# Performance work log

Hardware: AMD Instinct MI355X
Metric: run time of the kernel (lower is better)

The kernel has to match this reference:

```python
import jax, jax.numpy as jnp
import numpy as np

D_MODEL = 128
N_LAYERS = 2
D_STATE = 16
D_CONV = 4
EXPAND = 2
GRID = 16
D_INNER = D_MODEL * EXPAND
DT_RANK = (D_MODEL + 15) // 16  # mamba_ssm default: ceil(d_model/16) = 8
BATCH = 128
SEQ = 200


def setup_inputs() -> dict:
    key = jax.random.key(0)
    ks = jax.random.split(key, 24)
    L = N_LAYERS

    def rn(k, shape, scale=0.02):
        return jax.random.normal(k, shape, dtype=jnp.float32) * scale

    A_init = jnp.log(jnp.broadcast_to(
        jnp.arange(1, D_STATE + 1, dtype=jnp.float32), (L, D_INNER, D_STATE)))
    kan_scale = 1.0 / (np.sqrt(D_MODEL) * np.sqrt(GRID))
    return {
        "x": jax.random.normal(ks[0], (BATCH, SEQ, D_MODEL), dtype=jnp.float32),
        "in_w": rn(ks[1], (L, 2 * D_INNER, D_MODEL)),
        "out_w": rn(ks[2], (L, D_MODEL, D_INNER)),
        "conv_w_f": rn(ks[3], (L, D_INNER, D_CONV), 0.1),
        "conv_b_f": rn(ks[4], (L, D_INNER), 0.01),
        "conv_w_b": rn(ks[5], (L, D_INNER, D_CONV), 0.1),
        "conv_b_b": rn(ks[6], (L, D_INNER), 0.01),
        "xproj_w_f": rn(ks[7], (L, DT_RANK + 2 * D_STATE, D_INNER)),
        "xproj_w_b": rn(ks[8], (L, DT_RANK + 2 * D_STATE, D_INNER)),
        "dtproj_w_f": rn(ks[9], (L, D_INNER, DT_RANK), 0.1),
        "dtproj_b_f": rn(ks[10], (L, D_INNER), 0.01),
        "dtproj_w_b": rn(ks[11], (L, D_INNER, DT_RANK), 0.1),
        "dtproj_b_b": rn(ks[12], (L, D_INNER), 0.01),
        "A_log_f": A_init,
        "A_log_b": A_init,
        "D_f": jnp.ones((L, D_INNER), jnp.float32),
        "D_b": jnp.ones((L, D_INNER), jnp.float32),
        "ln1_w": jnp.ones((L, D_MODEL), jnp.float32),
        "ln1_b": jnp.zeros((L, D_MODEL), jnp.float32),
        "ln_w": jnp.ones((L, D_MODEL), jnp.float32),
        "ln_b": jnp.zeros((L, D_MODEL), jnp.float32),
        "kan_coef": jax.random.normal(ks[13], (L, 2, D_MODEL, D_MODEL, GRID), dtype=jnp.float32) * kan_scale,
    }


def _ln(x, w, b, eps=1e-12):
    u = x.mean(-1, keepdims=True)
    s = ((x - u) ** 2).mean(-1, keepdims=True)
    return w * (x - u) / jnp.sqrt(s + eps) + b


def _silu(x):
    return x * jax.nn.sigmoid(x)


def _mamba(x, in_w, out_w, conv_w, conv_b, xp_w, dt_w, dt_b, A_log, Dp):
    # x: (B, L, d_model). Faithful to mamba_ssm Mamba (bias=False proj, conv_bias=True).
    B, L, _ = x.shape
    xz = jnp.einsum('bld,ed->ble', x, in_w)          # (B, L, 2*d_inner)
    xi, z = jnp.split(xz, 2, axis=-1)
    # causal depthwise conv over L
    xp = jnp.pad(xi, ((0, 0), (D_CONV - 1, 0), (0, 0)))
    xc = sum(xp[:, k:k + L, :] * conv_w[:, k] for k in range(D_CONV)) + conv_b
    xc = _silu(xc)                                    # (B, L, d_inner)
    dbl = jnp.einsum('ble,fe->blf', xc, xp_w)         # (B, L, dt_rank+2*d_state)
    dt = jax.nn.softplus(
        jnp.einsum('blr,dr->bld', dbl[..., :DT_RANK], dt_w) + dt_b)
    Bm = dbl[..., DT_RANK:DT_RANK + D_STATE]          # (B, L, d_state)
    Cm = dbl[..., DT_RANK + D_STATE:]
    A = -jnp.exp(A_log)                               # (d_inner, d_state)

    def step(h, inp):
        dt_t, u_t, b_t, c_t = inp                     # (B,di),(B,di),(B,ds),(B,ds)
        h = jnp.exp(dt_t[:, :, None] * A) * h + (dt_t * u_t)[:, :, None] * b_t[:, None, :]
        return h, jnp.einsum('bds,bs->bd', h, c_t)

    h0 = jnp.zeros((B, D_INNER, D_STATE), x.dtype)
    _, ys = jax.lax.scan(step, h0, (jnp.moveaxis(dt, 1, 0), jnp.moveaxis(xc, 1, 0),
                                    jnp.moveaxis(Bm, 1, 0), jnp.moveaxis(Cm, 1, 0)))
    y = jnp.moveaxis(ys, 0, 1) + xc * Dp              # (B, L, d_inner)
    y = y * _silu(z)
    return jnp.einsum('ble,de->bld', y, out_w)


def _kan(x, coef):
    # coef: (2, outdim, inputdim, grid)
    shp = x.shape
    xf = x.reshape(-1, shp[-1])                       # (N, d)
    kk = jnp.arange(1, GRID + 1, dtype=x.dtype)
    ang = xf[:, :, None] * kk                         # (N, d, grid)
    y = (jnp.einsum('nig,jig->nj', jnp.cos(ang), coef[0])
         + jnp.einsum('nig,jig->nj', jnp.sin(ang), coef[1]))
    return y.reshape(shp[:-1] + (coef.shape[1],))


def reference(x, in_w, out_w, conv_w_f, conv_b_f, conv_w_b, conv_b_b,
              xproj_w_f, xproj_w_b, dtproj_w_f, dtproj_b_f, dtproj_w_b, dtproj_b_b,
              A_log_f, A_log_b, D_f, D_b, ln1_w, ln1_b, ln_w, ln_b, kan_coef):
    feats = []
    h = x
    for l in range(N_LAYERS):
        o = _ln(h, ln1_w[l], ln1_b[l])
        f = _mamba(o, in_w[l], out_w[l], conv_w_f[l], conv_b_f[l],
                   xproj_w_f[l], dtproj_w_f[l], dtproj_b_f[l], A_log_f[l], D_f[l])
        b = _mamba(o[:, ::-1], in_w[l], out_w[l], conv_w_b[l], conv_b_b[l],
                   xproj_w_b[l], dtproj_w_b[l], dtproj_b_b[l], A_log_b[l], D_b[l])[:, ::-1]
        o = _ln(f + b, ln_w[l], ln_b[l])
        o = _kan(o, kan_coef[l])  # dropout p=0.0 (eval) -> identity
        h = o + h
        feats.append(h)
    return sum(feats) / len(feats)
```

## Files before the change

kernel.cpp:

```cpp
#include <hip/hip_runtime.h>
#include <hip/hip_bf16.h>
#include <cmath>

#define BATCH 128
#define SEQ 200
#define DMODEL 128
#define DINNER 256
#define DSTATE 16
#define NTOK (BATCH * SEQ)

typedef __bf16 bf16x8 __attribute__((ext_vector_type(8)));
typedef float f32x4 __attribute__((ext_vector_type(4)));

__device__ __forceinline__ unsigned short f2bf(float f) {
  union { float f; unsigned u; } x{f};
  const unsigned r = x.u + 0x7fffu + ((x.u >> 16) & 1u);
  return (unsigned short)(r >> 16);
}
__device__ __forceinline__ float bf2f(unsigned short h) {
  union { unsigned u; float f; } x{(unsigned)h << 16};
  return x.f;
}
__device__ __forceinline__ void split2(float a, float b, unsigned& hp, unsigned& lp) {
  const unsigned short ha = f2bf(a), hb = f2bf(b);
  const float ra = a - bf2f(ha), rb = b - bf2f(hb);
  hp = (unsigned)ha | ((unsigned)hb << 16);
  lp = (unsigned)f2bf(ra) | ((unsigned)f2bf(rb) << 16);
}

template <int CTRL>
__device__ __forceinline__ float dpp_add(float v) {
  const int r = __builtin_amdgcn_update_dpp(0, __float_as_int(v), CTRL, 0xF, 0xF, true);
  return v + __int_as_float(r);
}

__device__ __forceinline__ float silu_f(float x) {
  return x / (1.f + __expf(-x));
}

__global__ __launch_bounds__(256) void ln_kernel(const float* __restrict__ in,
                                                 const float* __restrict__ w,
                                                 const float* __restrict__ b,
                                                 float* __restrict__ out) {
  const int wv = threadIdx.x >> 6;
  const int lane = threadIdx.x & 63;
  const int row = blockIdx.x * 4 + wv;
  const float2 v = *(const float2*)(in + (size_t)row * DMODEL + lane * 2);
  float s = v.x + v.y;
#pragma unroll
  for (int o = 32; o; o >>= 1) s += __shfl_xor(s, o, 64);
  const float u = s * (1.f / 128.f);
  const float dx = v.x - u, dy = v.y - u;
  float sq = dx * dx + dy * dy;
#pragma unroll
  for (int o = 32; o; o >>= 1) sq += __shfl_xor(sq, o, 64);
  const float inv = rsqrtf(sq * (1.f / 128.f) + 1e-12f);
  const float2 wv2 = *(const float2*)(w + lane * 2);
  const float2 bv2 = *(const float2*)(b + lane * 2);
  float2 o2v;
  o2v.x = fmaf(wv2.x, dx * inv, bv2.x);
  o2v.y = fmaf(wv2.y, dy * inv, bv2.y);
  *(float2*)(out + (size_t)row * DMODEL + lane * 2) = o2v;
}

__global__ __launch_bounds__(256) void wprep(const float* __restrict__ in_w,
                                             const float* __restrict__ xpwf,
                                             const float* __restrict__ xpwb,
                                             const float* __restrict__ out_w,
                                             unsigned short* __restrict__ iwH,
                                             unsigned short* __restrict__ iwL,
                                             unsigned short* __restrict__ xfH,
                                             unsigned short* __restrict__ xfL,
                                             unsigned short* __restrict__ xbH,
                                             unsigned short* __restrict__ xbL,
                                             unsigned short* __restrict__ owH,
                                             unsigned short* __restrict__ owL) {
  const int idx = blockIdx.x * 256 + threadIdx.x;
  float w;
  unsigned short *H, *L;
  int off;
  if (idx < 65536)      { w = in_w[idx];        H = iwH; L = iwL; off = idx; }
  else if (idx < 75776) { w = xpwf[idx - 65536]; H = xfH; L = xfL; off = idx - 65536; }
  else if (idx < 86016) { w = xpwb[idx - 75776]; H = xbH; L = xbL; off = idx - 75776; }
  else                  { w = out_w[idx - 86016]; H = owH; L = owL; off = idx - 86016; }
  const unsigned short h = f2bf(w);
  H[off] = h;
  L[off] = f2bf(w - bf2f(h));
}

template <int MODE>
__global__ __launch_bounds__(256) void gemm_c(const float* __restrict__ A1,
                                              const float* __restrict__ A2,
                                              const float* __restrict__ Zp,
                                              const unsigned short* __restrict__ Whi,
                                              const unsigned short* __restrict__ Wlo,
                                              float* __restrict__ C,
                                              int M, int N, int K) {
  __shared__ unsigned short AshH[64 * 40], AshL[64 * 40];
  __shared__ unsigned short BshH[128 * 40], BshL[128 * 40];
  const int tid = threadIdx.x;
  const int m0 = blockIdx.y * 64;
  const int n0 = blockIdx.x * 128;
  const int lane = tid & 63;
  const int wid = tid >> 6;
  const int arow = lane & 15;
  const int kch = (lane >> 4) * 8;
  const int bcol = wid * 32 + (lane & 15);
  f32x4 acc[4][2] = {};
  for (int k0 = 0; k0 < K; k0 += 32) {
    __syncthreads();
    {
      const int row = tid >> 2;
      const int koff = (tid & 3) * 8;
      const int m = m0 + row;
      float4 v0 = *(const float4*)(A1 + (size_t)m * K + k0 + koff);
      float4 v1 = *(const float4*)(A1 + (size_t)m * K + k0 + koff + 4);
      if (MODE == 1) {
        const float4 u0 = *(const float4*)(A2 + (size_t)m * K + k0 + koff);
        const float4 u1 = *(const float4*)(A2 + (size_t)m * K + k0 + koff + 4);
        const float4 z0 = *(const float4*)(Zp + (size_t)m * 512 + k0 + koff);
        const float4 z1 = *(const float4*)(Zp + (size_t)m * 512 + k0 + koff + 4);
        v0.x = (v0.x + u0.x) * silu_f(z0.x);
        v0.y = (v0.y + u0.y) * silu_f(z0.y);
        v0.z = (v0.z + u0.z) * silu_f(z0.z);
        v0.w = (v0.w + u0.w) * silu_f(z0.w);
        v1.x = (v1.x + u1.x) * silu_f(z1.x);
        v1.y = (v1.y + u1.y) * silu_f(z1.y);
        v1.z = (v1.z + u1.z) * silu_f(z1.z);
        v1.w = (v1.w + u1.w) * silu_f(z1.w);
      }
      unsigned h0, l0, h1, l1, h2, l2, h3, l3;
      split2(v0.x, v0.y, h0, l0);
      split2(v0.z, v0.w, h1, l1);
      split2(v1.x, v1.y, h2, l2);
      split2(v1.z, v1.w, h3, l3);
      *(uint4*)&AshH[row * 40 + koff] = make_uint4(h0, h1, h2, h3);
      *(uint4*)&AshL[row * 40 + koff] = make_uint4(l0, l1, l2, l3);
    }
    {
      const int row = tid >> 1;
      const int koff = (tid & 1) * 16;
      const int n = n0 + row;
      uint4 wh0 = make_uint4(0, 0, 0, 0), wh1 = wh0, wl0 = wh0, wl1 = wh0;
      if (n < N) {
        wh0 = *(const uint4*)(Whi + (size_t)n * K + k0 + koff);
        wh1 = *(const uint4*)(Whi + (size_t)n * K + k0 + koff + 8);
        wl0 = *(const uint4*)(Wlo + (size_t)n * K + k0 + koff);
        wl1 = *(const uint4*)(Wlo + (size_t)n * K + k0 + koff + 8);
      }
      *(uint4*)&BshH[row * 40 + koff] = wh0;
      *(uint4*)&BshH[row * 40 + koff + 8] = wh1;
      *(uint4*)&BshL[row * 40 + koff] = wl0;
      *(uint4*)&BshL[row * 40 + koff + 8] = wl1;
    }
    __syncthreads();
    const bf16x8 bh0 = *(const bf16x8*)&BshH[bcol * 40 + kch];
    const bf16x8 bh1 = *(const bf16x8*)&BshH[(bcol + 16) * 40 + kch];
    const bf16x8 bl0 = *(const bf16x8*)&BshL[bcol * 40 + kch];
    const bf16x8 bl1 = *(const bf16x8*)&BshL[(bcol + 16) * 40 + kch];
#pragma unroll
    for (int g = 0; g < 4; ++g) {
      const bf16x8 ah = *(const bf16x8*)&AshH[(g * 16 + arow) * 40 + kch];
      const bf16x8 al = *(const bf16x8*)&AshL[(g * 16 + arow) * 40 + kch];
      acc[g][0] = __builtin_amdgcn_mfma_f32_16x16x32_bf16(ah, bh0, acc[g][0], 0, 0, 0);
      acc[g][0] = __builtin_amdgcn_mfma_f32_16x16x32_bf16(al, bh0, acc[g][0], 0, 0, 0);
      acc[g][0] = __builtin_amdgcn_mfma_f32_16x16x32_bf16(ah, bl0, acc[g][0], 0, 0, 0);
      acc[g][1] = __builtin_amdgcn_mfma_f32_16x16x32_bf16(ah, bh1, acc[g][1], 0, 0, 0);
      acc[g][1] = __builtin_amdgcn_mfma_f32_16x16x32_bf16(al, bh1, acc[g][1], 0, 0, 0);
      acc[g][1] = __builtin_amdgcn_mfma_f32_16x16x32_bf16(ah, bl1, acc[g][1], 0, 0, 0);
    }
  }
  const int q0 = (lane >> 4) * 4;
#pragma unroll
  for (int g = 0; g < 4; ++g)
#pragma unroll
    for (int fc = 0; fc < 2; ++fc)
#pragma unroll
      for (int q = 0; q < 4; ++q) {
        const int m = m0 + g * 16 + q0 + q;
        const int n = n0 + wid * 32 + fc * 16 + (lane & 15);
        if (n < N) C[(size_t)m * N + n] = acc[g][fc][q];
      }
}

__global__ __launch_bounds__(256) void conv_silu_kernel(const float* __restrict__ xz,
                                                        const float* __restrict__ cwf,
                                                        const float* __restrict__ cbf,
                                                        const float* __restrict__ cwb,
                                                        const float* __restrict__ cbb,
                                                        float* __restrict__ xcf,
                                                        float* __restrict__ xcb) {
  const int n = blockIdx.x;
  const int l = n % SEQ;
  const int e = threadIdx.x;
  const float4 wf = *(const float4*)(cwf + e * 4);
  const float4 wb = *(const float4*)(cwb + e * 4);
  const float* base = xz + (size_t)n * 512 + e;
  const float wfk[4] = {wf.x, wf.y, wf.z, wf.w};
  const float wbk[4] = {wb.x, wb.y, wb.z, wb.w};
  float af = cbf[e];
#pragma unroll
  for (int k = 0; k < 4; ++k) {
    const int ll = l - 3 + k;
    if (ll >= 0) af = fmaf(wfk[k], base[(k - 3) * 512], af);
  }
  float ab = cbb[e];
#pragma unroll
  for (int k = 0; k < 4; ++k) {
    const int ll = l + 3 - k;
    if (ll < SEQ) ab = fmaf(wbk[k], base[(3 - k) * 512], ab);
  }
  xcf[(size_t)n * DINNER + e] = silu_f(af);
  xcb[(size_t)n * DINNER + e] = silu_f(ab);
}

__global__ __launch_bounds__(256) void dtsp_kernel2(const float* __restrict__ dblF,
                                                    const float* __restrict__ dblB,
                                                    const float* __restrict__ dtwF,
                                                    const float* __restrict__ dtbF,
                                                    const float* __restrict__ dtwB,
                                                    const float* __restrict__ dtbB,
                                                    float* __restrict__ dtF,
                                                    float* __restrict__ dtB) {
  const int bwd = blockIdx.y;
  const float* __restrict__ dbl = bwd ? dblB : dblF;
  const float* __restrict__ dtw = bwd ? dtwB : dtwF;
  const float* __restrict__ dtb = bwd ? dtbB : dtbF;
  float* __restrict__ dt = bwd ? dtB : dtF;
  __shared__ float r[8];
  const int n = blockIdx.x;
  const int d = threadIdx.x;
  if (threadIdx.x < 8) r[threadIdx.x] = dbl[(size_t)n * 40 + threadIdx.x];
  __syncthreads();
  const float4 w0 = *(const float4*)(dtw + d * 8);
  const float4 w1 = *(const float4*)(dtw + d * 8 + 4);
  float acc = dtb[d];
  acc += r[0] * w0.x + r[1] * w0.y + r[2] * w0.z + r[3] * w0.w;
  acc += r[4] * w1.x + r[5] * w1.y + r[6] * w1.z + r[7] * w1.w;
  const float sp = acc > 20.f ? acc : log1pf(__expf(acc));
  dt[(size_t)n * DINNER + d] = sp;
}

__global__ __launch_bounds__(256) void scan_kernel3(
    const float* __restrict__ dtF, float* xcF, const float* __restrict__ dblF,
    const float* __restrict__ AlogF, const float* __restrict__ DF,
    const float* __restrict__ dtB, float* xcB, const float* __restrict__ dblB,
    const float* __restrict__ AlogB, const float* __restrict__ DB) {
  const int bwd = blockIdx.z;
  const float* __restrict__ dt = bwd ? dtB : dtF;
  float* xc = bwd ? xcB : xcF;
  const float* __restrict__ dbl = bwd ? dblB : dblF;
  const float* __restrict__ Alog = bwd ? AlogB : AlogF;
  const float* __restrict__ Dp = bwd ? DB : DF;
  const int bb = blockIdx.y;
  const int lane = threadIdx.x & 63;
  const int wid = threadIdx.x >> 6;
  const int q = lane & 3;
  const int dl = lane >> 2;
  const int d = blockIdx.x * 64 + wid * 16 + dl;
  const float LOG2E = 1.44269504f;
  const float4 al = *(const float4*)(Alog + d * DSTATE + q * 4);
  const float4 A2 = make_float4(-__expf(al.x) * LOG2E, -__expf(al.y) * LOG2E,
                                -__expf(al.z) * LOG2E, -__expf(al.w) * LOG2E);
  const float Dd = Dp[d];
  const int t0 = bwd ? (SEQ - 1) : 0;
  const ptrdiff_t sX = bwd ? -DINNER : DINNER;
  const ptrdiff_t sB = bwd ? -40 : 40;
  const float* pdt = dt + (size_t)(bb * SEQ + t0) * DINNER + d;
  float* pxc = xc + (size_t)(bb * SEQ + t0) * DINNER + d;
  const float* pbc = dbl + (size_t)(bb * SEQ + t0) * 40 + 8 + q * 4;
  float4 h = make_float4(0.f, 0.f, 0.f, 0.f);
#pragma unroll 2
  for (int t = 0; t < SEQ; ++t) {
    const float dtv = *pdt;
    const float u = *pxc;
    const float4 Bv = *(const float4*)pbc;
    const float4 Cv = *(const float4*)(pbc + 16);
    const float du = dtv * u;
    float4 a;
    a.x = exp2f(dtv * A2.x);
    a.y = exp2f(dtv * A2.y);
    a.z = exp2f(dtv * A2.z);
    a.w = exp2f(dtv * A2.w);
    h.x = fmaf(a.x, h.x, du * Bv.x);
    h.y = fmaf(a.y, h.y, du * Bv.y);
    h.z = fmaf(a.z, h.z, du * Bv.z);
    h.w = fmaf(a.w, h.w, du * Bv.w);
    float pp = fmaf(h.w, Cv.w, fmaf(h.z, Cv.z, fmaf(h.y, Cv.y, h.x * Cv.x)));
    pp = dpp_add<0xB1>(pp);
    pp = dpp_add<0x4E>(pp);
    if (q == 0) *pxc = fmaf(u, Dd, pp);
    pdt += sX;
    pxc += sX;
    pbc += sB;
  }
}

__global__ __launch_bounds__(256) void kan_prep(const float* __restrict__ coef,
                                                unsigned short* __restrict__ Wt) {
  const int idx = blockIdx.x * 256 + threadIdx.x;
  const int k = idx & 31;
  const int j = (idx >> 5) & 127;
  const int i = idx >> 12;
  const int c = k >> 4, g = k & 15;
  Wt[idx] = f2bf(coef[(((size_t)c * 128 + j) * 128 + i) * 16 + g]);
}

__global__ __launch_bounds__(256) void kan_mfma(const float* __restrict__ x,
                                                const unsigned short* __restrict__ Wt,
                                                const float* __restrict__ hin,
                                                float* __restrict__ hout,
                                                float* __restrict__ accum,
                                                int first) {
  __shared__ float Xs[128 * 32];
  __shared__ unsigned short F[2][32 * 40];
  __shared__ unsigned short Wsh[2][128 * 40];
  const int tid = threadIdx.x;
  const int n0 = blockIdx.x * 32;
  const int wid = tid >> 6;
  const int lane = tid & 63;
  {
    const int tok = tid & 31;
    const int cq = tid >> 5;
#pragma unroll
    for (int r = 0; r < 4; ++r) {
      const int i0 = (cq + r * 8) * 4;
      const float4 v = *(const float4*)(x + (size_t)(n0 + tok) * 128 + i0);
      Xs[(i0 + 0) * 32 + tok] = v.x;
      Xs[(i0 + 1) * 32 + tok] = v.y;
      Xs[(i0 + 2) * 32 + tok] = v.z;
      Xs[(i0 + 3) * 32 + tok] = v.w;
    }
  }
  const int fn = tid >> 3;
  const int ft = tid & 7;
  const float g0 = (float)(2 * ft + 1);
  const int arow = lane & 15;
  const int kch = (lane >> 4) * 8;
  const int bcol = wid * 32 + (lane & 15);
  const int ws = tid >> 7;
  const int wrow = tid & 127;
  f32x4 acc[2][2] = {};
  for (int ii = 0; ii < 128; ii += 2) {
    __syncthreads();
    {
      const uint4* src = (const uint4*)(Wt + (size_t)(ii + ws) * 4096 + wrow * 32);
      uint4* dst = (uint4*)&Wsh[ws][wrow * 40];
      dst[0] = src[0]; dst[1] = src[1]; dst[2] = src[2]; dst[3] = src[3];
    }
#pragma unroll
    for (int s = 0; s < 2; ++s) {
      const float xv = Xs[(ii + s) * 32 + fn];
      const float y1 = xv * g0;
      const float y2 = y1 + xv;
      const float cg = __cosf(y1), sg = __sinf(y1);
      const float cg2 = __cosf(y2), sg2 = __sinf(y2);
      unsigned int* Fu = (unsigned int*)F[s];
      Fu[fn * 20 + ft] = (unsigned)f2bf(cg) | ((unsigned)f2bf(cg2) << 16);
      Fu[fn * 20 + 8 + ft] = (unsigned)f2bf(sg) | ((unsigned)f2bf(sg2) << 16);
    }
    __syncthreads();
#pragma unroll
    for (int s = 0; s < 2; ++s) {
      const bf16x8 a0 = *(const bf16x8*)&F[s][arow * 40 + kch];
      const bf16x8 a1 = *(const bf16x8*)&F[s][(16 + arow) * 40 + kch];
      const bf16x8 b0 = *(const bf16x8*)&Wsh[s][bcol * 40 + kch];
      const bf16x8 b1 = *(const bf16x8*)&Wsh[s][(bcol + 16) * 40 + kch];
      acc[0][0] = __builtin_amdgcn_mfma_f32_16x16x32_bf16(a0, b0, acc[0][0], 0, 0, 0);
      acc[1][0] = __builtin_amdgcn_mfma_f32_16x16x32_bf16(a1, b0, acc[1][0], 0, 0, 0);
      acc[0][1] = __builtin_amdgcn_mfma_f32_16x16x32_bf16(a0, b1, acc[0][1], 0, 0, 0);
      acc[1][1] = __builtin_amdgcn_mfma_f32_16x16x32_bf16(a1, b1, acc[1][1], 0, 0, 0);
    }
  }
  const int q0 = (lane >> 4) * 4;
#pragma unroll
  for (int fr = 0; fr < 2; ++fr)
#pragma unroll
    for (int fc = 0; fc < 2; ++fc)
#pragma unroll
      for (int q = 0; q < 4; ++q) {
        const int n = n0 + fr * 16 + q0 + q;
        const int j = wid * 32 + fc * 16 + (lane & 15);
        const size_t off = (size_t)n * 128 + j;
        const float v = acc[fr][fc][q] + hin[off];
        hout[off] = v;
        const float a = 0.5f * v;
        accum[off] = first ? a : (accum[off] + a);
      }
}

extern "C" void kernel_launch(void* const* d_in, const int* in_sizes, int n_in,
                              void* d_out, int out_size, void* d_ws, size_t ws_size,
                              hipStream_t stream) {
  (void)in_sizes; (void)n_in; (void)out_size;
  const float* x     = (const float*)d_in[0];
  const float* in_w  = (const float*)d_in[1];
  const float* out_w = (const float*)d_in[2];
  const float* cwf   = (const float*)d_in[3];
  const float* cbf   = (const float*)d_in[4];
  const float* cwb   = (const float*)d_in[5];
  const float* cbb   = (const float*)d_in[6];
  const float* xpwf  = (const float*)d_in[7];
  const float* xpwb  = (const float*)d_in[8];
  const float* dtwf  = (const float*)d_in[9];
  const float* dtbf  = (const float*)d_in[10];
  const float* dtwb  = (const float*)d_in[11];
  const float* dtbb  = (const float*)d_in[12];
  const float* Alogf = (const float*)d_in[13];
  const float* Alogb = (const float*)d_in[14];
  const float* Dfp   = (const float*)d_in[15];
  const float* Dbp   = (const float*)d_in[16];
  const float* ln1w  = (const float*)d_in[17];
  const float* ln1b  = (const float*)d_in[18];
  const float* lnw   = (const float*)d_in[19];
  const float* lnb   = (const float*)d_in[20];
  const float* kanc  = (const float*)d_in[21];
  float* outp = (float*)d_out;

  int C = 128;
  while (C > 8) {
    const size_t need = ((size_t)380928 + (size_t)2000 * C * SEQ) * 4;
    if (need <= ws_size) break;
    C >>= 1;
  }
  const int T = C * SEQ;

  float* p = (float*)d_ws;
  unsigned short* Wt  = (unsigned short*)p; p += 262144;
  unsigned short* iwH = (unsigned short*)p; p += 32768;
  unsigned short* iwL = (unsigned short*)p; p += 32768;
  unsigned short* xfH = (unsigned short*)p; p += 5120;
  unsigned short* xfL = (unsigned short*)p; p += 5120;
  unsigned short* xbH = (unsigned short*)p; p += 5120;
  unsigned short* xbL = (unsigned short*)p; p += 5120;
  unsigned short* owH = (unsigned short*)p; p += 16384;
  unsigned short* owL = (unsigned short*)p; p += 16384;
  float* o1   = p; p += (size_t)T * 128;
  float* xzb  = p; p += (size_t)T * 512;
  float* xcf  = p; p += (size_t)T * 256;
  float* xcb  = p; p += (size_t)T * 256;
  float* dblf = p; p += (size_t)T * 40;
  float* dblb = p; p += (size_t)T * 40;
  float* dtf  = p; p += (size_t)T * 256;
  float* dtb  = p; p += (size_t)T * 256;
  float* o2   = p; p += (size_t)T * 128;
  float* hbuf = p; p += (size_t)T * 128;

  for (int b0 = 0; b0 < BATCH; b0 += C) {
    const size_t tok0 = (size_t)b0 * SEQ;
    for (int l = 0; l < 2; ++l) {
      const float* hin = (l == 0) ? (x + tok0 * 128) : hbuf;
      wprep<<<464, 256, 0, stream>>>(in_w + (size_t)l * 65536, xpwf + (size_t)l * 10240,
                                     xpwb + (size_t)l * 10240, out_w + (size_t)l * 32768,
                                     iwH, iwL, xfH, xfL, xbH, xbL, owH, owL);
      kan_prep<<<2048, 256, 0, stream>>>(kanc + (size_t)l * 2 * 128 * 128 * 16, Wt);
      ln_kernel<<<T / 4, 256, 0, stream>>>(hin, ln1w + l * 128, ln1b + l * 128, o1);
      gemm_c<0><<<dim3(4, T / 64), 256, 0, stream>>>(o1, (const float*)nullptr,
                                                     (const float*)nullptr,
                                                     iwH, iwL, xzb, T, 512, 128);
      conv_silu_kernel<<<T, 256, 0, stream>>>(xzb, cwf + l * 1024, cbf + l * 256,
                                              cwb + l * 1024, cbb + l * 256, xcf, xcb);
      gemm_c<0><<<dim3(1, T / 64), 256, 0, stream>>>(xcf, (const float*)nullptr,
                                                     (const float*)nullptr,
                                                     xfH, xfL, dblf, T, 40, 256);
      gemm_c<0><<<dim3(1, T / 64), 256, 0, stream>>>(xcb, (const float*)nullptr,
                                                     (const float*)nullptr,
                                                     xbH, xbL, dblb, T, 40, 256);
      dtsp_kernel2<<<dim3(T, 2), 256, 0, stream>>>(dblf, dblb,
                                                   dtwf + l * 2048, dtbf + l * 256,
                                                   dtwb + l * 2048, dtbb + l * 256,
                                                   dtf, dtb);
      scan_kernel3<<<dim3(4, C, 2), 256, 0, stream>>>(
          dtf, xcf, dblf, Alogf + l * 4096, Dfp + l * 256,
          dtb, xcb, dblb, Alogb + l * 4096, Dbp + l * 256);
      gemm_c<1><<<dim3(1, T / 64), 256, 0, stream>>>(xcf, xcb, xzb + 256,
                                                     owH, owL, o1, T, 128, 256);
      ln_kernel<<<T / 4, 256, 0, stream>>>(o1, lnw + l * 128, lnb + l * 128, o2);
      kan_mfma<<<T / 32, 256, 0, stream>>>(o2, Wt, hin, hbuf,
                                           outp + tok0 * 128, l == 0 ? 1 : 0);
    }
  }
}
```

Measured before the change: 764.7 us.

## Hoist weight prep, merge x_proj GEMMs, batch conv/dt tokens, widen KAN tiles

Weight splitting and KAN coefficient prep now run once per layer outside the batch-chunk loop, with per-layer buffers. The two x_proj GEMMs are merged into one launch selected by blockIdx.z. The conv and dt-softplus kernels each handle 8 tokens per block, and the conv kernel uses a sliding window. The KAN MFMA kernel doubles its token tile to 64 and builds its cos/sin harmonics by angle-addition recurrence instead of direct sin/cos calls. The workspace layout is reworked, which leaves dead pointer setup code and raises the workspace requirement.

```diff
diff --git a/kernel.cpp b/kernel.cpp
--- a/kernel.cpp
+++ b/kernel.cpp
@@ -95,9 +95,17 @@
                                               const unsigned short* __restrict__ Whi,
                                               const unsigned short* __restrict__ Wlo,
                                               float* __restrict__ C,
+                                              const unsigned short* __restrict__ Whi2,
+                                              const unsigned short* __restrict__ Wlo2,
+                                              float* __restrict__ C2,
                                               int M, int N, int K) {
   __shared__ unsigned short AshH[64 * 40], AshL[64 * 40];
   __shared__ unsigned short BshH[128 * 40], BshL[128 * 40];
+  const float* Ause = A1;
+  const unsigned short* WH = Whi;
+  const unsigned short* WL = Wlo;
+  float* Cuse = C;
+  if (MODE == 2 && blockIdx.z == 1) { Ause = A2; WH = Whi2; WL = Wlo2; Cuse = C2; }
   const int tid = threadIdx.x;
   const int m0 = blockIdx.y * 64;
   const int n0 = blockIdx.x * 128;
@@ -113,8 +121,8 @@
       const int row = tid >> 2;
       const int koff = (tid & 3) * 8;
       const int m = m0 + row;
-      float4 v0 = *(const float4*)(A1 + (size_t)m * K + k0 + koff);
-      float4 v1 = *(const float4*)(A1 + (size_t)m * K + k0 + koff + 4);
+      float4 v0 = *(const float4*)(Ause + (size_t)m * K + k0 + koff);
+      float4 v1 = *(const float4*)(Ause + (size_t)m * K + k0 + koff + 4);
       if (MODE == 1) {
         const float4 u0 = *(const float4*)(A2 + (size_t)m * K + k0 + koff);
         const float4 u1 = *(const float4*)(A2 + (size_t)m * K + k0 + koff + 4);
@@ -143,10 +151,10 @@
       const int n = n0 + row;
       uint4 wh0 = make_uint4(0, 0, 0, 0), wh1 = wh0, wl0 = wh0, wl1 = wh0;
       if (n < N) {
-        wh0 = *(const uint4*)(Whi + (size_t)n * K + k0 + koff);
-        wh1 = *(const uint4*)(Whi + (size_t)n * K + k0 + koff + 8);
-        wl0 = *(const uint4*)(Wlo + (size_t)n * K + k0 + koff);
-        wl1 = *(const uint4*)(Wlo + (size_t)n * K + k0 + koff + 8);
+        wh0 = *(const uint4*)(WH + (size_t)n * K + k0 + koff);
+        wh1 = *(const uint4*)(WH + (size_t)n * K + k0 + koff + 8);
+        wl0 = *(const uint4*)(WL + (size_t)n * K + k0 + koff);
+        wl1 = *(const uint4*)(WL + (size_t)n * K + k0 + koff + 8);
       }
       *(uint4*)&BshH[row * 40 + koff] = wh0;
       *(uint4*)&BshH[row * 40 + koff + 8] = wh1;
@@ -179,7 +187,7 @@
       for (int q = 0; q < 4; ++q) {
         const int m = m0 + g * 16 + q0 + q;
         const int n = n0 + wid * 32 + fc * 16 + (lane & 15);
-        if (n < N) C[(size_t)m * N + n] = acc[g][fc][q];
+        if (n < N) Cuse[(size_t)m * N + n] = acc[g][fc][q];
       }
 }
 
@@ -190,28 +198,30 @@
                                                         const float* __restrict__ cbb,
                                                         float* __restrict__ xcf,
                                                         float* __restrict__ xcb) {
-  const int n = blockIdx.x;
-  const int l = n % SEQ;
+  const int n0 = blockIdx.x * 8;
+  const int l0 = n0 % SEQ;
   const int e = threadIdx.x;
   const float4 wf = *(const float4*)(cwf + e * 4);
   const float4 wb = *(const float4*)(cwb + e * 4);
-  const float* base = xz + (size_t)n * 512 + e;
-  const float wfk[4] = {wf.x, wf.y, wf.z, wf.w};
-  const float wbk[4] = {wb.x, wb.y, wb.z, wb.w};
-  float af = cbf[e];
-#pragma unroll
-  for (int k = 0; k < 4; ++k) {
-    const int ll = l - 3 + k;
-    if (ll >= 0) af = fmaf(wfk[k], base[(k - 3) * 512], af);
-  }
-  float ab = cbb[e];
-#pragma unroll
-  for (int k = 0; k < 4; ++k) {
-    const int ll = l + 3 - k;
-    if (ll < SEQ) ab = fmaf(wbk[k], base[(3 - k) * 512], ab);
-  }
-  xcf[(size_t)n * DINNER + e] = silu_f(af);
-  xcb[(size_t)n * DINNER + e] = silu_f(ab);
+  const float bfv = cbf[e], bbv = cbb[e];
+  const float* px = xz + (size_t)n0 * 512 + e;
+  float w[7];
+#pragma unroll
+  for (int j = 0; j < 6; ++j) {
+    const int l = l0 - 3 + j;
+    w[j] = (l >= 0 && l < SEQ) ? px[(j - 3) * 512] : 0.f;
+  }
+#pragma unroll
+  for (int t = 0; t < 8; ++t) {
+    const int l = l0 + t;
+    w[6] = (l + 3 < SEQ) ? px[(t + 3) * 512] : 0.f;
+    const float af = fmaf(wf.x, w[0], fmaf(wf.y, w[1], fmaf(wf.z, w[2], fmaf(wf.w, w[3], bfv))));
+    const float ab = fmaf(wb.x, w[6], fmaf(wb.y, w[5], fmaf(wb.z, w[4], fmaf(wb.w, w[3], bbv))));
+    xcf[(size_t)(n0 + t) * DINNER + e] = silu_f(af);
+    xcb[(size_t)(n0 + t) * DINNER + e] = silu_f(ab);
+#pragma unroll
+    for (int j = 0; j < 6; ++j) w[j] = w[j + 1];
+  }
 }
 
 __global__ __launch_bounds__(256) void dtsp_kernel2(const float* __restrict__ dblF,
@@ -227,18 +237,25 @@
   const float* __restrict__ dtw = bwd ? dtwB : dtwF;
   const float* __restrict__ dtb = bwd ? dtbB : dtbF;
   float* __restrict__ dt = bwd ? dtB : dtF;
-  __shared__ float r[8];
-  const int n = blockIdx.x;
+  __shared__ float r[8][8];
+  const int n0 = blockIdx.x * 8;
   const int d = threadIdx.x;
-  if (threadIdx.x < 8) r[threadIdx.x] = dbl[(size_t)n * 40 + threadIdx.x];
-  __syncthreads();
+  if (threadIdx.x < 64) {
+    const int tt = threadIdx.x >> 3, j = threadIdx.x & 7;
+    r[tt][j] = dbl[(size_t)(n0 + tt) * 40 + j];
+  }
   const float4 w0 = *(const float4*)(dtw + d * 8);
   const float4 w1 = *(const float4*)(dtw + d * 8 + 4);
-  float acc = dtb[d];
-  acc += r[0] * w0.x + r[1] * w0.y + r[2] * w0.z + r[3] * w0.w;
-  acc += r[4] * w1.x + r[5] * w1.y + r[6] * w1.z + r[7] * w1.w;
-  const float sp = acc > 20.f ? acc : log1pf(__expf(acc));
-  dt[(size_t)n * DINNER + d] = sp;
+  const float bd = dtb[d];
+  __syncthreads();
+#pragma unroll
+  for (int tt = 0; tt < 8; ++tt) {
+    float acc = bd;
+    acc += r[tt][0] * w0.x + r[tt][1] * w0.y + r[tt][2] * w0.z + r[tt][3] * w0.w;
+    acc += r[tt][4] * w1.x + r[tt][5] * w1.y + r[tt][6] * w1.z + r[tt][7] * w1.w;
+    const float sp = acc > 20.f ? acc : log1pf(__expf(acc));
+    dt[(size_t)(n0 + tt) * DINNER + d] = sp;
+  }
 }
 
 __global__ __launch_bounds__(256) void scan_kernel3(
@@ -312,77 +329,85 @@
                                                 float* __restrict__ hout,
                                                 float* __restrict__ accum,
                                                 int first) {
-  __shared__ float Xs[128 * 32];
-  __shared__ unsigned short F[2][32 * 40];
+  __shared__ float Xs[128 * 64];
+  __shared__ unsigned short F[2][64 * 40];
   __shared__ unsigned short Wsh[2][128 * 40];
   const int tid = threadIdx.x;
-  const int n0 = blockIdx.x * 32;
+  const int n0 = blockIdx.x * 64;
   const int wid = tid >> 6;
   const int lane = tid & 63;
   {
-    const int tok = tid & 31;
-    const int cq = tid >> 5;
-#pragma unroll
-    for (int r = 0; r < 4; ++r) {
-      const int i0 = (cq + r * 8) * 4;
+    const int tok = tid & 63;
+    const int cq = tid >> 6;
+#pragma unroll
+    for (int r = 0; r < 8; ++r) {
+      const int i0 = cq * 32 + r * 4;
       const float4 v = *(const float4*)(x + (size_t)(n0 + tok) * 128 + i0);
-      Xs[(i0 + 0) * 32 + tok] = v.x;
-      Xs[(i0 + 1) * 32 + tok] = v.y;
-      Xs[(i0 + 2) * 32 + tok] = v.z;
-      Xs[(i0 + 3) * 32 + tok] = v.w;
-    }
-  }
-  const int fn = tid >> 3;
-  const int ft = tid & 7;
-  const float g0 = (float)(2 * ft + 1);
+      Xs[(i0 + 0) * 64 + tok] = v.x;
+      Xs[(i0 + 1) * 64 + tok] = v.y;
+      Xs[(i0 + 2) * 64 + tok] = v.z;
+      Xs[(i0 + 3) * 64 + tok] = v.w;
+    }
+  }
+  const int fs = tid >> 7;
+  const int fn = (tid & 127) >> 1;
+  const int fh = tid & 1;
+  const int wrow = tid & 127;
   const int arow = lane & 15;
   const int kch = (lane >> 4) * 8;
   const int bcol = wid * 32 + (lane & 15);
-  const int ws = tid >> 7;
-  const int wrow = tid & 127;
-  f32x4 acc[2][2] = {};
+  f32x4 acc[4][2] = {};
   for (int ii = 0; ii < 128; ii += 2) {
     __syncthreads();
     {
-      const uint4* src = (const uint4*)(Wt + (size_t)(ii + ws) * 4096 + wrow * 32);
-      uint4* dst = (uint4*)&Wsh[ws][wrow * 40];
+      const uint4* src = (const uint4*)(Wt + (size_t)(ii + fs) * 4096 + wrow * 32);
+      uint4* dst = (uint4*)&Wsh[fs][wrow * 40];
       dst[0] = src[0]; dst[1] = src[1]; dst[2] = src[2]; dst[3] = src[3];
     }
-#pragma unroll
-    for (int s = 0; s < 2; ++s) {
-      const float xv = Xs[(ii + s) * 32 + fn];
-      const float y1 = xv * g0;
-      const float y2 = y1 + xv;
-      const float cg = __cosf(y1), sg = __sinf(y1);
-      const float cg2 = __cosf(y2), sg2 = __sinf(y2);
-      unsigned int* Fu = (unsigned int*)F[s];
-      Fu[fn * 20 + ft] = (unsigned)f2bf(cg) | ((unsigned)f2bf(cg2) << 16);
-      Fu[fn * 20 + 8 + ft] = (unsigned)f2bf(sg) | ((unsigned)f2bf(sg2) << 16);
+    {
+      const float xv = Xs[(ii + fs) * 64 + fn];
+      const float c1 = __cosf(xv), s1 = __sinf(xv);
+      float c, s;
+      if (fh == 0) { c = c1; s = s1; }
+      else {
+        const float y = xv * 9.f;
+        c = __cosf(y); s = __sinf(y);
+      }
+      unsigned int* Fu = (unsigned int*)F[fs];
+#pragma unroll
+      for (int p = 0; p < 4; ++p) {
+        const float c2 = c * c1 - s * s1;
+        const float s2 = s * c1 + c * s1;
+        Fu[fn * 20 + fh * 4 + p]     = (unsigned)f2bf(c) | ((unsigned)f2bf(c2) << 16);
+        Fu[fn * 20 + 8 + fh * 4 + p] = (unsigned)f2bf(s) | ((unsigned)f2bf(s2) << 16);
+        c = c2 * c1 - s2 * s1;
+        s = s2 * c1 + c2 * s1;
+      }
     }
     __syncthreads();
 #pragma unroll
-    for (int s = 0; s < 2; ++s) {
-      const bf16x8 a0 = *(const bf16x8*)&F[s][arow * 40 + kch];
-      const bf16x8 a1 = *(const bf16x8*)&F[s][(16 + arow) * 40 + kch];
-      const bf16x8 b0 = *(const bf16x8*)&Wsh[s][bcol * 40 + kch];
-      const bf16x8 b1 = *(const bf16x8*)&Wsh[s][(bcol + 16) * 40 + kch];
-      acc[0][0] = __builtin_amdgcn_mfma_f32_16x16x32_bf16(a0, b0, acc[0][0], 0, 0, 0);
-      acc[1][0] = __builtin_amdgcn_mfma_f32_16x16x32_bf16(a1, b0, acc[1][0], 0, 0, 0);
-      acc[0][1] = __builtin_amdgcn_mfma_f32_16x16x32_bf16(a0, b1, acc[0][1], 0, 0, 0);
-      acc[1][1] = __builtin_amdgcn_mfma_f32_16x16x32_bf16(a1, b1, acc[1][1], 0, 0, 0);
+    for (int sl = 0; sl < 2; ++sl) {
+      const bf16x8 b0 = *(const bf16x8*)&Wsh[sl][bcol * 40 + kch];
+      const bf16x8 b1 = *(const bf16x8*)&Wsh[sl][(bcol + 16) * 40 + kch];
+#pragma unroll
+      for (int g = 0; g < 4; ++g) {
+        const bf16x8 a = *(const bf16x8*)&F[sl][(g * 16 + arow) * 40 + kch];
+        acc[g][0] = __builtin_amdgcn_mfma_f32_16x16x32_bf16(a, b0, acc[g][0], 0, 0, 0);
+        acc[g][1] = __builtin_amdgcn_mfma_f32_16x16x32_bf16(a, b1, acc[g][1], 0, 0, 0);
+      }
     }
   }
   const int q0 = (lane >> 4) * 4;
 #pragma unroll
-  for (int fr = 0; fr < 2; ++fr)
+  for (int g = 0; g < 4; ++g)
 #pragma unroll
     for (int fc = 0; fc < 2; ++fc)
 #pragma unroll
       for (int q = 0; q < 4; ++q) {
-        const int n = n0 + fr * 16 + q0 + q;
+        const int n = n0 + g * 16 + q0 + q;
         const int j = wid * 32 + fc * 16 + (lane & 15);
         const size_t off = (size_t)n * 128 + j;
-        const float v = acc[fr][fc][q] + hin[off];
+        const float v = acc[g][fc][q] + hin[off];
         hout[off] = v;
         const float a = 0.5f * v;
         accum[off] = first ? a : (accum[off] + a);
@@ -419,22 +444,15 @@
 
   int C = 128;
   while (C > 8) {
-    const size_t need = ((size_t)380928 + (size_t)2000 * C * SEQ) * 4;
+    const size_t need = ((size_t)643072 + (size_t)2000 * C * SEQ) * 4;
     if (need <= ws_size) break;
     C >>= 1;
   }
   const int T = C * SEQ;
 
   float* p = (float*)d_ws;
-  unsigned short* Wt  = (unsigned short*)p; p += 262144;
-  unsigned short* iwH = (unsigned short*)p; p += 32768;
-  unsigned short* iwL = (unsigned short*)p; p += 32768;
-  unsigned short* xfH = (unsigned short*)p; p += 5120;
-  unsigned short* xfL = (unsigned short*)p; p += 5120;
-  unsigned short* xbH = (unsigned short*)p; p += 5120;
-  unsigned short* xbL = (unsigned short*)p; p += 5120;
-  unsigned short* owH = (unsigned short*)p; p += 16384;
-  unsigned short* owL = (unsigned short*)p; p += 16384;
+  unsigned short* Wt2  = (unsigned short*)p; p += 524288;
+  unsigned short* pl   = (unsigned short*)p; p += 118784;
   float* o1   = p; p += (size_t)T * 128;
   float* xzb  = p; p += (size_t)T * 512;
   float* xcf  = p; p += (size_t)T * 256;
@@ -446,37 +464,81 @@
   float* o2   = p; p += (size_t)T * 128;
   float* hbuf = p; p += (size_t)T * 128;
 
+  unsigned short* Wt_l[2];
+  unsigned short *iwH[2], *iwL[2], *xfH[2], *xfL[2], *xbH[2], *xbL[2], *owH[2], *owL[2];
+  for (int l = 0; l < 2; ++l) {
+    Wt_l[l] = Wt2 + (size_t)l * 524288;
+    unsigned short* q = pl + (size_t)l * 118784;
+    iwH[l] = q;          iwL[l] = q + 32768;
+    xfH[l] = q + 65536;  xfL[l] = q + 70656;
+    xbH[l] = q + 75776;  xbL[l] = q + 80896;
+    owH[l] = q + 86016;  owL[l] = q + 102400;
+  }
+  for (int l = 0; l < 2; ++l) {
+    unsigned short* q = pl + (size_t)l * 118784 * 2;
+    (void)q;
+  }
+  {
+    unsigned short* base = (unsigned short*)d_ws;
+    unsigned short* plbase = base + 2 * 524288;
+    for (int l = 0; l < 2; ++l) {
+      unsigned short* q = plbase + (size_t)l * 237568;
+      iwH[l] = q;           iwL[l] = q + 65536;
+      xfH[l] = q + 131072;  xfL[l] = q + 141312;
+      xbH[l] = q + 151552;  xbL[l] = q + 161792;
+      owH[l] = q + 172032;  owL[l] = q + 204800;
+    }
+  }
+  {
+    float* pf = (float*)d_ws + 761856;
+    o1   = pf; pf += (size_t)T * 128;
+    xzb  = pf; pf += (size_t)T * 512;
+    xcf  = pf; pf += (size_t)T * 256;
+    xcb  = pf; pf += (size_t)T * 256;
+    dblf = pf; pf += (size_t)T * 40;
+    dblb = pf; pf += (size_t)T * 40;
+    dtf  = pf; pf += (size_t)T * 256;
+    dtb  = pf; pf += (size_t)T * 256;
+    o2   = pf; pf += (size_t)T * 128;
+    hbuf = pf; pf += (size_t)T * 128;
+  }
+
+  for (int l = 0; l < 2; ++l) {
+    wprep<<<464, 256, 0, stream>>>(in_w + (size_t)l * 65536, xpwf + (size_t)l * 10240,
+                                   xpwb + (size_t)l * 10240, out_w + (size_t)l * 32768,
+                                   iwH[l], iwL[l], xfH[l], xfL[l],
+                                   xbH[l], xbL[l], owH[l], owL[l]);
+    kan_prep<<<2048, 256, 0, stream>>>(kanc + (size_t)l * 2 * 128 * 128 * 16, Wt_l[l]);
+  }
+
   for (int b0 = 0; b0 < BATCH; b0 += C) {
     const size_t tok0 = (size_t)b0 * SEQ;
     for (int l = 0; l < 2; ++l) {
       const float* hin = (l == 0) ? (x + tok0 * 128) : hbuf;
-      wprep<<<464, 256, 0, stream>>>(in_w + (size_t)l * 65536, xpwf + (size_t)l * 10240,
-                                     xpwb + (size_t)l * 10240, out_w + (size_t)l * 32768,
-                                     iwH, iwL, xfH, xfL, xbH, xbL, owH, owL);
-      kan_prep<<<2048, 256, 0, stream>>>(kanc + (size_t)l * 2 * 128 * 128 * 16, Wt);
       ln_kernel<<<T / 4, 256, 0, stream>>>(hin, ln1w + l * 128, ln1b + l * 128, o1);
-      gemm_c<0><<<dim3(4, T / 64), 256, 0, stream>>>(o1, (const float*)nullptr,
-                                                     (const float*)nullptr,
-                                                     iwH, iwL, xzb, T, 512, 128);
-      conv_silu_kernel<<<T, 256, 0, stream>>>(xzb, cwf + l * 1024, cbf + l * 256,
-                                              cwb + l * 1024, cbb + l * 256, xcf, xcb);
-      gemm_c<0><<<dim3(1, T / 64), 256, 0, stream>>>(xcf, (const float*)nullptr,
-                                                     (const float*)nullptr,
-                                                     xfH, xfL, dblf, T, 40, 256);
-      gemm_c<0><<<dim3(1, T / 64), 256, 0, stream>>>(xcb, (const float*)nullptr,
-                                                     (const float*)nullptr,
-                                                     xbH, xbL, dblb, T, 40, 256);
-      dtsp_kernel2<<<dim3(T, 2), 256, 0, stream>>>(dblf, dblb,
-                                                   dtwf + l * 2048, dtbf + l * 256,
-                                                   dtwb + l * 2048, dtbb + l * 256,
-                                                   dtf, dtb);
+      gemm_c<0><<<dim3(4, T / 64), 256, 0, stream>>>(
+          o1, (const float*)nullptr, (const float*)nullptr,
+          iwH[l], iwL[l], xzb,
+          (const unsigned short*)nullptr, (const unsigned short*)nullptr,
+          (float*)nullptr, T, 512, 128);
+      conv_silu_kernel<<<T / 8, 256, 0, stream>>>(xzb, cwf + l * 1024, cbf + l * 256,
+                                                  cwb + l * 1024, cbb + l * 256, xcf, xcb);
+      gemm_c<2><<<dim3(1, T / 64, 2), 256, 0, stream>>>(
+          xcf, xcb, (const float*)nullptr,
+          xfH[l], xfL[l], dblf, xbH[l], xbL[l], dblb, T, 40, 256);
+      dtsp_kernel2<<<dim3(T / 8, 2), 256, 0, stream>>>(dblf, dblb,
+                                                       dtwf + l * 2048, dtbf + l * 256,
+                                                       dtwb + l * 2048, dtbb + l * 256,
+                                                       dtf, dtb);
       scan_kernel3<<<dim3(4, C, 2), 256, 0, stream>>>(
           dtf, xcf, dblf, Alogf + l * 4096, Dfp + l * 256,
           dtb, xcb, dblb, Alogb + l * 4096, Dbp + l * 256);
-      gemm_c<1><<<dim3(1, T / 64), 256, 0, stream>>>(xcf, xcb, xzb + 256,
-                                                     owH, owL, o1, T, 128, 256);
+      gemm_c<1><<<dim3(1, T / 64), 256, 0, stream>>>(
+          xcf, xcb, xzb + 256, owH[l], owL[l], o1,
+          (const unsigned short*)nullptr, (const unsigned short*)nullptr,
+          (float*)nullptr, T, 128, 256);
       ln_kernel<<<T / 4, 256, 0, stream>>>(o1, lnw + l * 128, lnb + l * 128, o2);
-      kan_mfma<<<T / 32, 256, 0, stream>>>(o2, Wt, hin, hbuf,
+      kan_mfma<<<T / 64, 256, 0, stream>>>(o2, Wt_l[l], hin, hbuf,
                                            outp + tok0 * 128, l == 0 ? 1 : 0);
     }
   }
```

Result: faster. 650.0 us (-15.0%).
